# Optimization experiments

Measured on AMD Instinct MI355X. Metric: run time of the kernel, lower is better.

Reference implementation:

```python
import jax, jax.numpy as jnp
import numpy as np


def setup_inputs() -> dict:
    key = jax.random.key(0)
    k1, k2, k3 = jax.random.split(key, 3)
    B, C, T = 8, 256, 4096
    H, K = 512, 4
    x = jax.random.normal(k1, (B, C, T), dtype=jnp.float32)
    W = jax.random.normal(k2, (H, C * K), dtype=jnp.float32) * 0.02
    b = jax.random.normal(k3, (H,), dtype=jnp.float32) * 0.02
    return {"x": x, "W": W, "b": b}


def reference(x, W, b):
    # Causal conv1d equivalent of the per-step Linear loop (stride=1).
    # Original flattens window as view(B, C*K): channel-major -> W[h, c*K + k].
    B, C, T = x.shape
    H = W.shape[0]
    K = W.shape[1] // C
    kernel = W.reshape(H, C, K)  # OIH layout
    out = jax.lax.conv_general_dilated(
        x, kernel,
        window_strides=(1,),
        padding=[(K - 1, 0)],  # left-pad only => causal
        dimension_numbers=("NCH", "OIH", "NCH"),
    )
    return out + b[None, :, None]  # (B, H, T)
```

## Files before the change

kernel.cpp:

```cpp
#include <hip/hip_runtime.h>
#include <hip/hip_bf16.h>


#define Bb 8
#define Cc 256
#define Tt 4096
#define Hh 512
#define Kk 4

typedef __attribute__((ext_vector_type(8))) short bf16x8;
typedef __attribute__((ext_vector_type(4))) float f32x4;

#define WS_XT_OFF   0
#define WS_WT_OFF   16777216
#define WS_ZERO_OFF 17825792
#define WS_NEEDED   17825856ULL

__device__ __forceinline__ void gload16(const void* g, void* l) {
    __builtin_amdgcn_global_load_lds(
        (const __attribute__((address_space(1))) void*)g,
        (__attribute__((address_space(3))) void*)l, 16, 0, 0);
}

__global__ __launch_bounds__(256) void wt_prep_kernel(const float* __restrict__ W,
                                                      __hip_bfloat16* __restrict__ Wt,
                                                      float* __restrict__ zeros) {
    int n = blockIdx.x * 256 + threadIdx.x;
    int c = n & 255;
    int h = (n >> 8) & 511;
    int k = n >> 17;
    Wt[n] = __float2bfloat16(W[h * (Cc * Kk) + c * Kk + k]);
    if (blockIdx.x == 0 && threadIdx.x < 16) zeros[threadIdx.x] = 0.f;
}

__global__ __launch_bounds__(256) void xt_prep_kernel(const float* __restrict__ x,
                                                      __hip_bfloat16* __restrict__ xT) {
    __shared__ __hip_bfloat16 tile[64][66];
    const int t0 = blockIdx.x * 64, c0 = blockIdx.y * 64, b = blockIdx.z;
    const int lt = threadIdx.x & 63, lw = threadIdx.x >> 6;
#pragma unroll
    for (int i = 0; i < 16; ++i) {
        int cc = lw + i * 4;
        tile[cc][lt] = __float2bfloat16(x[((size_t)(b * Cc + c0 + cc)) * Tt + t0 + lt]);
    }
    __syncthreads();
#pragma unroll
    for (int i = 0; i < 16; ++i) {
        int tt = lw + i * 4;
        xT[((size_t)(b * Tt + t0 + tt)) * Cc + c0 + lt] = tile[lt][tt];
    }
}

#define LDS_A_OFF 0
#define LDS_B_OFF 32768
#define LDS_TOTAL 41984

__global__ __launch_bounds__(256) void conv_mfma_kernel(const __hip_bfloat16* __restrict__ xT,
                                                        const __hip_bfloat16* __restrict__ Wt,
                                                        const float* __restrict__ bias,
                                                        const float* __restrict__ zeros,
                                                        float* __restrict__ out) {
    __shared__ __align__(1024) char smem[LDS_TOTAL];
    const int tid  = threadIdx.x;
    const int lane = tid & 63;
    const int wave = tid >> 6;
    const int wr = wave >> 1, wc = wave & 1;
    const int l15 = lane & 15, lg = lane >> 4;
    const int t0 = blockIdx.x * 128, h0 = blockIdx.y * 128, b = blockIdx.z;

    f32x4 acc[4][4] = {};

    for (int step = 0; step < 8; ++step) {
        const int c0 = step * 32;
        if (step) __syncthreads();

#pragma unroll
        for (int inst = 0; inst < 8; ++inst) {
            int s = tid + inst * 256;
            int k = s >> 9, rem = s & 511;
            int row = rem >> 2, q = rem & 3;
            const char* src = (const char*)Wt +
                (((size_t)(k * Hh + h0 + row)) * Cc + c0 + q * 8) * 2;
            char* dst = smem + LDS_A_OFF + (wave * 64 + inst * 256) * 16;
            gload16(src, dst);
        }
#pragma unroll
        for (int inst = 0; inst < 2; ++inst) {
            int s = tid + inst * 256;
            int row = s >> 2, q = s & 3;
            int tg = t0 - 3 + row;
            const void* src = (tg >= 0)
                ? (const void*)((const char*)xT + (((size_t)b * Tt + tg) * Cc + c0 + q * 8) * 2)
                : (const void*)zeros;
            char* dst = smem + LDS_B_OFF + (wave * 64 + inst * 256) * 16;
            gload16(src, dst);
        }
        if (wave == 0) {
            int s = tid + 512;
            int row = s >> 2, q = s & 3;
            int tg = t0 - 3 + row;
            const void* src = (row < 131)
                ? (const void*)((const char*)xT + (((size_t)b * Tt + tg) * Cc + c0 + q * 8) * 2)
                : (const void*)zeros;
            char* dst = smem + LDS_B_OFF + 512 * 16;
            gload16(src, dst);
        }
        __syncthreads();

#pragma unroll
        for (int k = 0; k < 4; ++k) {
            bf16x8 af[4], bfr[4];
#pragma unroll
            for (int i = 0; i < 4; ++i) {
                int row = wr * 64 + i * 16 + l15;
                af[i] = *(const bf16x8*)(smem + LDS_A_OFF + k * 8192 + row * 64 + lg * 16);
            }
#pragma unroll
            for (int j = 0; j < 4; ++j) {
                int row = wc * 64 + j * 16 + l15 + k;
                bfr[j] = *(const bf16x8*)(smem + LDS_B_OFF + row * 64 + lg * 16);
            }
#pragma unroll
            for (int i = 0; i < 4; ++i)
#pragma unroll
                for (int j = 0; j < 4; ++j)
                    acc[i][j] = __builtin_amdgcn_mfma_f32_16x16x32_bf16(af[i], bfr[j], acc[i][j], 0, 0, 0);
        }
    }

#pragma unroll
    for (int i = 0; i < 4; ++i) {
        int hb = h0 + wr * 64 + i * 16 + lg * 4;
        float4 bs = *(const float4*)&bias[hb];
        const float* bsp = (const float*)&bs;
#pragma unroll
        for (int q = 0; q < 4; ++q) {
            int h = hb + q;
#pragma unroll
            for (int j = 0; j < 4; ++j) {
                int t = t0 + wc * 64 + j * 16 + l15;
                out[((size_t)(b * Hh + h)) * Tt + t] = acc[i][j][q] + bsp[q];
            }
        }
    }
}

#define TT 256
#define HT 8
#define CT 4
__global__ __launch_bounds__(256) void conv1d_f32_kernel(
    const float* __restrict__ x, const float* __restrict__ W,
    const float* __restrict__ bias, float* __restrict__ out)
{
    const int tid = threadIdx.x;
    const int t0 = blockIdx.x * TT;
    const int h0 = blockIdx.y * HT;
    const int b  = blockIdx.z;
    __shared__ float xs[CT][TT + Kk];
    float acc[HT];
#pragma unroll
    for (int h = 0; h < HT; ++h) acc[h] = 0.f;
    const float* xb = x + (size_t)b * Cc * Tt;
    for (int c0 = 0; c0 < Cc; c0 += CT) {
        __syncthreads();
#pragma unroll
        for (int cc = 0; cc < CT; ++cc)
            for (int j = tid; j < TT + Kk - 1; j += 256) {
                int idx = t0 - (Kk - 1) + j;
                xs[cc][j] = (idx >= 0) ? xb[(size_t)(c0 + cc) * Tt + idx] : 0.f;
            }
        __syncthreads();
#pragma unroll
        for (int cc = 0; cc < CT; ++cc) {
            float xv[Kk];
#pragma unroll
            for (int k = 0; k < Kk; ++k) xv[k] = xs[cc][tid + k];
#pragma unroll
            for (int h = 0; h < HT; ++h) {
                const float* wp = W + (size_t)(h0 + h) * (Cc * Kk) + (size_t)(c0 + cc) * Kk;
#pragma unroll
                for (int k = 0; k < Kk; ++k) acc[h] += wp[k] * xv[k];
            }
        }
    }
#pragma unroll
    for (int h = 0; h < HT; ++h)
        out[((size_t)b * Hh + (h0 + h)) * Tt + t0 + tid] = acc[h] + bias[h0 + h];
}

extern "C" void kernel_launch(void* const* d_in, const int* in_sizes, int n_in,
                              void* d_out, int out_size, void* d_ws, size_t ws_size,
                              hipStream_t stream) {
    const float* x    = (const float*)d_in[0];
    const float* W    = (const float*)d_in[1];
    const float* bias = (const float*)d_in[2];
    float* out        = (float*)d_out;

    if (ws_size >= WS_NEEDED) {
        __hip_bfloat16* xT = (__hip_bfloat16*)((char*)d_ws + WS_XT_OFF);
        __hip_bfloat16* Wt = (__hip_bfloat16*)((char*)d_ws + WS_WT_OFF);
        float* zeros       = (float*)((char*)d_ws + WS_ZERO_OFF);

        wt_prep_kernel<<<dim3((Kk * Hh * Cc) / 256), dim3(256), 0, stream>>>(W, Wt, zeros);
        xt_prep_kernel<<<dim3(Tt / 64, Cc / 64, Bb), dim3(256), 0, stream>>>(x, xT);
        conv_mfma_kernel<<<dim3(Tt / 128, Hh / 128, Bb), dim3(256), 0, stream>>>(xT, Wt, bias, zeros, out);
    } else {
        conv1d_f32_kernel<<<dim3(Tt / TT, Hh / HT, Bb), dim3(256), 0, stream>>>(x, W, bias, out);
    }
}
```

Baseline: 59.08 us.

## Triple-buffer LDS pipeline with 512-thread blocks and larger time tiles

```diff
diff --git a/kernel.cpp b/kernel.cpp
--- a/kernel.cpp
+++ b/kernel.cpp
@@ -14,7 +14,7 @@
 #define WS_XT_OFF   0
 #define WS_WT_OFF   16777216
 #define WS_ZERO_OFF 17825792
-#define WS_NEEDED   17825856ULL
+#define WS_NEEDED   17826816ULL
 
 __device__ __forceinline__ void gload16(const void* g, void* l) {
     __builtin_amdgcn_global_load_lds(
@@ -30,7 +30,7 @@
     int h = (n >> 8) & 511;
     int k = n >> 17;
     Wt[n] = __float2bfloat16(W[h * (Cc * Kk) + c * Kk + k]);
-    if (blockIdx.x == 0 && threadIdx.x < 16) zeros[threadIdx.x] = 0.f;
+    if (blockIdx.x == 0) zeros[threadIdx.x] = 0.f;
 }
 
 __global__ __launch_bounds__(256) void xt_prep_kernel(const float* __restrict__ x,
@@ -51,81 +51,99 @@
     }
 }
 
-#define LDS_A_OFF 0
-#define LDS_B_OFF 32768
-#define LDS_TOTAL 41984
-
-__global__ __launch_bounds__(256) void conv_mfma_kernel(const __hip_bfloat16* __restrict__ xT,
-                                                        const __hip_bfloat16* __restrict__ Wt,
-                                                        const float* __restrict__ bias,
-                                                        const float* __restrict__ zeros,
-                                                        float* __restrict__ out) {
+#define BUF_BYTES 49664
+#define B_OFF     32768
+#define LDS_TOTAL (3 * BUF_BYTES)
+
+#define STG_A(s2, i) gload16(asrc[i] + (s2) * 64, smem + ((s2) % 3) * BUF_BYTES + adst[i])
+#define STG_B(s2, i) gload16(bsrc[i] + (s2) * 64, smem + ((s2) % 3) * BUF_BYTES + bdst[i])
+
+#define PHASE(s, k, DOSTAGE) do {                                                          \
+    const char* bufp = smem + ((s) % 3) * BUF_BYTES;                                       \
+    bf16x8 af[4], bfr[4];                                                                  \
+    _Pragma("unroll") for (int i = 0; i < 4; ++i)                                          \
+        af[i] = *(const bf16x8*)(bufp + (k) * 8192 + aoff_rd + i * 256);                   \
+    _Pragma("unroll") for (int j = 0; j < 4; ++j)                                          \
+        bfr[j] = *(const bf16x8*)(bufp + boff_rd + ((j) * 16 + (k)) * 16);                 \
+    DOSTAGE;                                                                               \
+    __builtin_amdgcn_s_barrier();                                                          \
+    asm volatile("s_waitcnt lgkmcnt(0)" ::: "memory");                                     \
+    __builtin_amdgcn_sched_barrier(0);                                                     \
+    __builtin_amdgcn_s_setprio(1);                                                         \
+    _Pragma("unroll") for (int i = 0; i < 4; ++i)                                          \
+        _Pragma("unroll") for (int j = 0; j < 4; ++j)                                      \
+            acc[i][j] = __builtin_amdgcn_mfma_f32_16x16x32_bf16(af[i], bfr[j],             \
+                                                                acc[i][j], 0, 0, 0);       \
+    __builtin_amdgcn_s_setprio(0);                                                         \
+} while (0)
+
+__global__ __launch_bounds__(512, 2) void conv_mfma_kernel(
+    const __hip_bfloat16* __restrict__ xT,
+    const __hip_bfloat16* __restrict__ Wt,
+    const float* __restrict__ bias,
+    const float* __restrict__ zeros,
+    float* __restrict__ out)
+{
     __shared__ __align__(1024) char smem[LDS_TOTAL];
     const int tid  = threadIdx.x;
     const int lane = tid & 63;
     const int wave = tid >> 6;
-    const int wr = wave >> 1, wc = wave & 1;
+    const int wr = wave >> 2, wc = wave & 3;
     const int l15 = lane & 15, lg = lane >> 4;
-    const int t0 = blockIdx.x * 128, h0 = blockIdx.y * 128, b = blockIdx.z;
+    const int t0 = blockIdx.x * 256;
+    const int h0 = blockIdx.y * 128;
+    const int b  = blockIdx.z;
+
+    const char* asrc[4];
+    int adst[4];
+#pragma unroll
+    for (int i = 0; i < 4; ++i) {
+        int sA = tid + i * 512;
+        int k = sA >> 9, cg = (sA >> 7) & 3, h = sA & 127;
+        asrc[i] = (const char*)Wt + (((size_t)(k * Hh + h0 + h)) * Cc + cg * 8) * 2;
+        adst[i] = sA * 16;
+    }
+    const char* bsrc[3];
+    int bdst[3];
+#pragma unroll
+    for (int i = 0; i < 3; ++i) {
+        int sB = tid + i * 512;
+        if (i == 2 && tid >= 32) sB = tid;
+        int cg = sB / 264, r = sB - cg * 264;
+        int tg = t0 - 3 + r;
+        bool oob = (r > 258) || (tg < 0);
+        bsrc[i] = oob ? (const char*)zeros
+                      : (const char*)xT + (((size_t)(b * Tt + tg)) * Cc + cg * 8) * 2;
+        bdst[i] = B_OFF + sB * 16;
+    }
 
     f32x4 acc[4][4] = {};
-
-    for (int step = 0; step < 8; ++step) {
-        const int c0 = step * 32;
-        if (step) __syncthreads();
-
-#pragma unroll
-        for (int inst = 0; inst < 8; ++inst) {
-            int s = tid + inst * 256;
-            int k = s >> 9, rem = s & 511;
-            int row = rem >> 2, q = rem & 3;
-            const char* src = (const char*)Wt +
-                (((size_t)(k * Hh + h0 + row)) * Cc + c0 + q * 8) * 2;
-            char* dst = smem + LDS_A_OFF + (wave * 64 + inst * 256) * 16;
-            gload16(src, dst);
-        }
-#pragma unroll
-        for (int inst = 0; inst < 2; ++inst) {
-            int s = tid + inst * 256;
-            int row = s >> 2, q = s & 3;
-            int tg = t0 - 3 + row;
-            const void* src = (tg >= 0)
-                ? (const void*)((const char*)xT + (((size_t)b * Tt + tg) * Cc + c0 + q * 8) * 2)
-                : (const void*)zeros;
-            char* dst = smem + LDS_B_OFF + (wave * 64 + inst * 256) * 16;
-            gload16(src, dst);
-        }
-        if (wave == 0) {
-            int s = tid + 512;
-            int row = s >> 2, q = s & 3;
-            int tg = t0 - 3 + row;
-            const void* src = (row < 131)
-                ? (const void*)((const char*)xT + (((size_t)b * Tt + tg) * Cc + c0 + q * 8) * 2)
-                : (const void*)zeros;
-            char* dst = smem + LDS_B_OFF + 512 * 16;
-            gload16(src, dst);
-        }
-        __syncthreads();
-
-#pragma unroll
-        for (int k = 0; k < 4; ++k) {
-            bf16x8 af[4], bfr[4];
-#pragma unroll
-            for (int i = 0; i < 4; ++i) {
-                int row = wr * 64 + i * 16 + l15;
-                af[i] = *(const bf16x8*)(smem + LDS_A_OFF + k * 8192 + row * 64 + lg * 16);
-            }
-#pragma unroll
-            for (int j = 0; j < 4; ++j) {
-                int row = wc * 64 + j * 16 + l15 + k;
-                bfr[j] = *(const bf16x8*)(smem + LDS_B_OFF + row * 64 + lg * 16);
-            }
-#pragma unroll
-            for (int i = 0; i < 4; ++i)
-#pragma unroll
-                for (int j = 0; j < 4; ++j)
-                    acc[i][j] = __builtin_amdgcn_mfma_f32_16x16x32_bf16(af[i], bfr[j], acc[i][j], 0, 0, 0);
-        }
+    const int aoff_rd = lg * 2048 + (wr * 64 + l15) * 16;
+    const int boff_rd = B_OFF + lg * 4224 + (wc * 64 + l15) * 16;
+
+#pragma unroll
+    for (int i = 0; i < 4; ++i) STG_A(0, i);
+#pragma unroll
+    for (int i = 0; i < 3; ++i) STG_B(0, i);
+#pragma unroll
+    for (int i = 0; i < 4; ++i) STG_A(1, i);
+#pragma unroll
+    for (int i = 0; i < 3; ++i) STG_B(1, i);
+    asm volatile("s_waitcnt vmcnt(7)" ::: "memory");
+    __builtin_amdgcn_s_barrier();
+
+#pragma unroll
+    for (int s = 0; s < 8; ++s) {
+        PHASE(s, 0, if (s < 6) { STG_A(s + 2, 0); STG_A(s + 2, 1); });
+        __builtin_amdgcn_s_barrier();
+        PHASE(s, 1, if (s < 6) { STG_A(s + 2, 2); STG_A(s + 2, 3); });
+        __builtin_amdgcn_s_barrier();
+        PHASE(s, 2, if (s < 6) { STG_B(s + 2, 0); STG_B(s + 2, 1); });
+        __builtin_amdgcn_s_barrier();
+        PHASE(s, 3, if (s < 6) { STG_B(s + 2, 2); });
+        if (s < 6)       asm volatile("s_waitcnt vmcnt(7)" ::: "memory");
+        else if (s == 6) asm volatile("s_waitcnt vmcnt(0)" ::: "memory");
+        if (s < 7) __builtin_amdgcn_s_barrier();
     }
 
 #pragma unroll
@@ -135,11 +153,10 @@
         const float* bsp = (const float*)&bs;
 #pragma unroll
         for (int q = 0; q < 4; ++q) {
-            int h = hb + q;
 #pragma unroll
             for (int j = 0; j < 4; ++j) {
                 int t = t0 + wc * 64 + j * 16 + l15;
-                out[((size_t)(b * Hh + h)) * Tt + t] = acc[i][j][q] + bsp[q];
+                out[((size_t)(b * Hh + hb + q)) * Tt + t] = acc[i][j][q] + bsp[q];
             }
         }
     }
@@ -203,7 +220,7 @@
 
         wt_prep_kernel<<<dim3((Kk * Hh * Cc) / 256), dim3(256), 0, stream>>>(W, Wt, zeros);
         xt_prep_kernel<<<dim3(Tt / 64, Cc / 64, Bb), dim3(256), 0, stream>>>(x, xT);
-        conv_mfma_kernel<<<dim3(Tt / 128, Hh / 128, Bb), dim3(256), 0, stream>>>(xT, Wt, bias, zeros, out);
+        conv_mfma_kernel<<<dim3(Tt / 256, Hh / 128, Bb), dim3(512), 0, stream>>>(xT, Wt, bias, zeros, out);
     } else {
         conv1d_f32_kernel<<<dim3(Tt / TT, Hh / HT, Bb), dim3(256), 0, stream>>>(x, W, bias, out);
     }
```

Result: slower. 65.90 us (+11.5%).

## Double-buffer conv MFMA kernel with 32x32x16 tiles and swizzled block order

Applied to the files above, without the earlier changes.

```diff
diff --git a/kernel.cpp b/kernel.cpp
--- a/kernel.cpp
+++ b/kernel.cpp
@@ -8,13 +8,13 @@
 #define Hh 512
 #define Kk 4
 
-typedef __attribute__((ext_vector_type(8))) short bf16x8;
-typedef __attribute__((ext_vector_type(4))) float f32x4;
+typedef __attribute__((ext_vector_type(8)))  short bf16x8;
+typedef __attribute__((ext_vector_type(16))) float f32x16;
 
 #define WS_XT_OFF   0
 #define WS_WT_OFF   16777216
 #define WS_ZERO_OFF 17825792
-#define WS_NEEDED   17825856ULL
+#define WS_NEEDED   17826816ULL
 
 __device__ __forceinline__ void gload16(const void* g, void* l) {
     __builtin_amdgcn_global_load_lds(
@@ -30,7 +30,7 @@
     int h = (n >> 8) & 511;
     int k = n >> 17;
     Wt[n] = __float2bfloat16(W[h * (Cc * Kk) + c * Kk + k]);
-    if (blockIdx.x == 0 && threadIdx.x < 16) zeros[threadIdx.x] = 0.f;
+    if (blockIdx.x == 0) zeros[threadIdx.x] = 0.f;
 }
 
 __global__ __launch_bounds__(256) void xt_prep_kernel(const float* __restrict__ x,
@@ -51,95 +51,97 @@
     }
 }
 
-#define LDS_A_OFF 0
-#define LDS_B_OFF 32768
-#define LDS_TOTAL 41984
-
-__global__ __launch_bounds__(256) void conv_mfma_kernel(const __hip_bfloat16* __restrict__ xT,
-                                                        const __hip_bfloat16* __restrict__ Wt,
-                                                        const float* __restrict__ bias,
-                                                        const float* __restrict__ zeros,
-                                                        float* __restrict__ out) {
-    __shared__ __align__(1024) char smem[LDS_TOTAL];
+#define BK        16
+#define NSTEPS    (Cc / BK)
+#define A_BYTES   16384
+#define BUF_BYTES 24576
+
+__global__ __launch_bounds__(256, 3) void conv_mfma_kernel(
+    const __hip_bfloat16* __restrict__ xT,
+    const __hip_bfloat16* __restrict__ Wt,
+    const float* __restrict__ bias,
+    const float* __restrict__ zeros,
+    float* __restrict__ out)
+{
+    __shared__ __align__(1024) char smem[2 * BUF_BYTES];
     const int tid  = threadIdx.x;
     const int lane = tid & 63;
     const int wave = tid >> 6;
     const int wr = wave >> 1, wc = wave & 1;
-    const int l15 = lane & 15, lg = lane >> 4;
-    const int t0 = blockIdx.x * 128, h0 = blockIdx.y * 128, b = blockIdx.z;
-
-    f32x4 acc[4][4] = {};
-
-    for (int step = 0; step < 8; ++step) {
-        const int c0 = step * 32;
-        if (step) __syncthreads();
-
-#pragma unroll
-        for (int inst = 0; inst < 8; ++inst) {
-            int s = tid + inst * 256;
-            int k = s >> 9, rem = s & 511;
-            int row = rem >> 2, q = rem & 3;
-            const char* src = (const char*)Wt +
-                (((size_t)(k * Hh + h0 + row)) * Cc + c0 + q * 8) * 2;
-            char* dst = smem + LDS_A_OFF + (wave * 64 + inst * 256) * 16;
-            gload16(src, dst);
-        }
-#pragma unroll
-        for (int inst = 0; inst < 2; ++inst) {
-            int s = tid + inst * 256;
-            int row = s >> 2, q = s & 3;
-            int tg = t0 - 3 + row;
-            const void* src = (tg >= 0)
-                ? (const void*)((const char*)xT + (((size_t)b * Tt + tg) * Cc + c0 + q * 8) * 2)
-                : (const void*)zeros;
-            char* dst = smem + LDS_B_OFF + (wave * 64 + inst * 256) * 16;
-            gload16(src, dst);
-        }
-        if (wave == 0) {
-            int s = tid + 512;
-            int row = s >> 2, q = s & 3;
-            int tg = t0 - 3 + row;
-            const void* src = (row < 131)
-                ? (const void*)((const char*)xT + (((size_t)b * Tt + tg) * Cc + c0 + q * 8) * 2)
-                : (const void*)zeros;
-            char* dst = smem + LDS_B_OFF + 512 * 16;
-            gload16(src, dst);
+    const int l31 = lane & 31, lh = lane >> 5;
+
+    const int flat = blockIdx.x + 32 * (blockIdx.y + 4 * blockIdx.z);
+    const int nf   = (flat & 7) * 128 + (flat >> 3);
+    const int t0 = (nf & 31) * 128;
+    const int h0 = ((nf >> 5) & 3) * 128;
+    const int b  = nf >> 7;
+
+    const char* asrc[4]; int adst[4];
+#pragma unroll
+    for (int i = 0; i < 4; ++i) {
+        int s = tid + i * 256;
+        int k = s >> 8, h = (s >> 1) & 127, ks = s & 1;
+        asrc[i] = (const char*)Wt + (((size_t)(k * Hh + h0 + h)) * Cc + ks * 8) * 2;
+        adst[i] = s * 16;
+    }
+    const char* bsrc[2]; int bdst[2];
+#pragma unroll
+    for (int i = 0; i < 2; ++i) {
+        int s = tid + i * 256;
+        int t = s >> 1, ks = s & 1;
+        int tg = t0 - 3 + t;
+        bool valid = (t <= 130) && (tg >= 0);
+        bsrc[i] = valid ? (const char*)xT + (((size_t)(b * Tt + tg)) * Cc + ks * 8) * 2
+                        : (const char*)zeros;
+        bdst[i] = A_BYTES + s * 16;
+    }
+
+    const int aoff = wr * 2048 + l31 * 32 + lh * 16;
+    const int boff = A_BYTES + wc * 2048 + l31 * 32 + lh * 16;
+
+    f32x16 acc[2][2] = {};
+
+#pragma unroll
+    for (int i = 0; i < 4; ++i) { gload16(asrc[i], smem + adst[i]); asrc[i] += BK * 2; }
+#pragma unroll
+    for (int i = 0; i < 2; ++i) { gload16(bsrc[i], smem + bdst[i]); bsrc[i] += BK * 2; }
+    __syncthreads();
+
+    int cur = 0;
+    for (int s = 0; s < NSTEPS; ++s) {
+        const char* bufp = smem + cur * BUF_BYTES;
+        char* nxtp = smem + (cur ^ 1) * BUF_BYTES;
+        if (s < NSTEPS - 1) {
+#pragma unroll
+            for (int i = 0; i < 4; ++i) { gload16(asrc[i], nxtp + adst[i]); asrc[i] += BK * 2; }
+#pragma unroll
+            for (int i = 0; i < 2; ++i) { gload16(bsrc[i], nxtp + bdst[i]); bsrc[i] += BK * 2; }
+        }
+#pragma unroll
+        for (int k = 0; k < 4; ++k) {
+            bf16x8 a0 = *(const bf16x8*)(bufp + k * 4096 + aoff);
+            bf16x8 a1 = *(const bf16x8*)(bufp + k * 4096 + 1024 + aoff);
+            bf16x8 b0 = *(const bf16x8*)(bufp + boff + k * 32);
+            bf16x8 b1 = *(const bf16x8*)(bufp + boff + 1024 + k * 32);
+            acc[0][0] = __builtin_amdgcn_mfma_f32_32x32x16_bf16(a0, b0, acc[0][0], 0, 0, 0);
+            acc[0][1] = __builtin_amdgcn_mfma_f32_32x32x16_bf16(a0, b1, acc[0][1], 0, 0, 0);
+            acc[1][0] = __builtin_amdgcn_mfma_f32_32x32x16_bf16(a1, b0, acc[1][0], 0, 0, 0);
+            acc[1][1] = __builtin_amdgcn_mfma_f32_32x32x16_bf16(a1, b1, acc[1][1], 0, 0, 0);
         }
         __syncthreads();
-
-#pragma unroll
-        for (int k = 0; k < 4; ++k) {
-            bf16x8 af[4], bfr[4];
-#pragma unroll
-            for (int i = 0; i < 4; ++i) {
-                int row = wr * 64 + i * 16 + l15;
-                af[i] = *(const bf16x8*)(smem + LDS_A_OFF + k * 8192 + row * 64 + lg * 16);
-            }
-#pragma unroll
-            for (int j = 0; j < 4; ++j) {
-                int row = wc * 64 + j * 16 + l15 + k;
-                bfr[j] = *(const bf16x8*)(smem + LDS_B_OFF + row * 64 + lg * 16);
-            }
-#pragma unroll
-            for (int i = 0; i < 4; ++i)
-#pragma unroll
-                for (int j = 0; j < 4; ++j)
-                    acc[i][j] = __builtin_amdgcn_mfma_f32_16x16x32_bf16(af[i], bfr[j], acc[i][j], 0, 0, 0);
-        }
-    }
-
-#pragma unroll
-    for (int i = 0; i < 4; ++i) {
-        int hb = h0 + wr * 64 + i * 16 + lg * 4;
-        float4 bs = *(const float4*)&bias[hb];
-        const float* bsp = (const float*)&bs;
-#pragma unroll
-        for (int q = 0; q < 4; ++q) {
-            int h = hb + q;
-#pragma unroll
-            for (int j = 0; j < 4; ++j) {
-                int t = t0 + wc * 64 + j * 16 + l15;
-                out[((size_t)(b * Hh + h)) * Tt + t] = acc[i][j][q] + bsp[q];
+        cur ^= 1;
+    }
+
+#pragma unroll
+    for (int i = 0; i < 2; ++i) {
+#pragma unroll
+        for (int j = 0; j < 2; ++j) {
+#pragma unroll
+            for (int r = 0; r < 16; ++r) {
+                int hl = (r & 3) + 8 * (r >> 2) + 4 * lh;
+                int h  = h0 + wr * 64 + i * 32 + hl;
+                int t  = t0 + wc * 64 + j * 32 + l31;
+                out[((size_t)(b * Hh + h)) * Tt + t] = acc[i][j][r] + bias[h];
             }
         }
     }
```

New measurement: 69.98 us. +18.5%, slower.
